# Kernel tuning notes

Hardware: AMD Instinct MI355X
Metric: run time of the kernel (lower is better)

The kernel has to match this reference:

```python
import jax, jax.numpy as jnp
import numpy as np

B, S, H = 1, 2048, 1024
E, INTER, TOP_K = 8, 2048, 2
ALPHA, LIMIT = 1.702, 7.0


def setup_inputs() -> dict:
    key = jax.random.key(0)
    ks = jax.random.split(key, 7)
    sc = 0.02
    return {
        'hidden_states': jax.random.normal(ks[0], (B, S, H), jnp.float32),
        'router_w': jax.random.normal(ks[1], (H, E), jnp.float32) * sc,
        'router_b': jax.random.normal(ks[2], (E,), jnp.float32) * sc,
        'gate_up_proj': jax.random.normal(ks[3], (E, H, 2 * INTER), jnp.float32) * sc,
        'gate_up_bias': jax.random.normal(ks[4], (E, 2 * INTER), jnp.float32) * sc,
        'down_proj': jax.random.normal(ks[5], (E, INTER, H), jnp.float32) * sc,
        'down_bias': jax.random.normal(ks[6], (E, H), jnp.float32) * sc,
    }


def reference(hidden_states, router_w, router_b, gate_up_proj, gate_up_bias, down_proj, down_bias):
    x = hidden_states  # [B,S,H]
    # router: top-k over expert logits, softmax over selected logits (gpt-oss style)
    logits = jnp.einsum('bsh,he->bse', x, router_w) + router_b
    top_vals, top_idx = jax.lax.top_k(logits, TOP_K)          # [B,S,K]
    topk_weights = jax.nn.softmax(top_vals, axis=-1)          # [B,S,K]
    # dense per-expert gate_up GEMM (dispatch is identity on 1 device)
    gu = jnp.einsum('bsh,ehn->besn', x, gate_up_proj)         # [B,E,S,2I]
    gu = gu + gate_up_bias[None, :, None, :]
    gate = jnp.minimum(gu[..., :INTER], LIMIT)
    up = jnp.clip(gu[..., INTER:], -LIMIT, LIMIT)
    glu = gate * jax.nn.sigmoid(gate * ALPHA)
    act = (up + 1.0) * glu                                    # [B,E,S,I]
    down = jnp.einsum('besl,elh->besh', act, down_proj)       # [B,E,S,H]
    down = down + down_bias[None, :, None, :]
    # combine: gather each token's K selected expert outputs, weight and sum
    down_bseh = jnp.transpose(down, (0, 2, 1, 3))             # [B,S,E,H]
    idx = jnp.broadcast_to(top_idx[..., None], (B, S, TOP_K, H))
    sel = jnp.take_along_axis(down_bseh, idx, axis=2)         # [B,S,K,H]
    return (sel * topk_weights[..., None]).sum(axis=2)        # [B,S,H]
```

## Files before the change

kernel.cpp:

```cpp
#include <hip/hip_runtime.h>
#include <hip/hip_bf16.h>
#include <math.h>

#define S 2048
#define H 1024
#define NE 8
#define INTER 2048
#define ALPHA 1.702f
#define LIMIT 7.0f

typedef __bf16 bf16x8 __attribute__((ext_vector_type(8)));
typedef float f32x4 __attribute__((ext_vector_type(4)));

#define WS_COUNTS 0
#define WS_SLOTS  4096
#define WS_W      (WS_SLOTS + NE*S*4)
#define WS_XB     (WS_W + 2*S*4)
#define WS_ACT    (WS_XB + (size_t)S*H*2)

static __device__ __forceinline__ unsigned short f2bf(float f) {
    union { __hip_bfloat16 h; unsigned short u; } cv;
    cv.h = __float2bfloat16(f);
    return cv.u;
}

static __device__ __forceinline__ void gload16(const void* g, void* l) {
    __builtin_amdgcn_global_load_lds(
        (const __attribute__((address_space(1))) unsigned int*)(unsigned long long)g,
        (__attribute__((address_space(3))) unsigned int*)(unsigned int)(unsigned long long)l,
        16, 0, 0);
}

__global__ __launch_bounds__(64) void router_conv(
    const float* __restrict__ x, const float* __restrict__ rw,
    const float* __restrict__ rb, int* __restrict__ counts,
    int* __restrict__ slots, float* __restrict__ slot_w,
    unsigned short* __restrict__ xb)
{
    int tok = blockIdx.x;
    int lane = threadIdx.x;
    const float4* xr = (const float4*)(x + (size_t)tok * H);
    ushort4* xo = (ushort4*)(xb + (size_t)tok * H);
    float acc[NE];
#pragma unroll
    for (int e = 0; e < NE; ++e) acc[e] = 0.f;
#pragma unroll
    for (int p = 0; p < H / 256; ++p) {
        int idx = p * 64 + lane;
        float4 v = xr[idx];
        ushort4 o;
        o.x = f2bf(v.x); o.y = f2bf(v.y); o.z = f2bf(v.z); o.w = f2bf(v.w);
        xo[idx] = o;
        const float* wr = rw + (size_t)idx * 4 * NE;
#pragma unroll
        for (int e = 0; e < NE; ++e)
            acc[e] += v.x * wr[e] + v.y * wr[NE + e] + v.z * wr[2 * NE + e] + v.w * wr[3 * NE + e];
    }
#pragma unroll
    for (int e = 0; e < NE; ++e) {
#pragma unroll
        for (int off = 32; off > 0; off >>= 1)
            acc[e] += __shfl_down(acc[e], off);
    }
    if (lane == 0) {
        float v[NE];
#pragma unroll
        for (int e = 0; e < NE; ++e) v[e] = acc[e] + rb[e];
        int i1 = 0; float v1 = v[0];
#pragma unroll
        for (int e = 1; e < NE; ++e) if (v[e] > v1) { v1 = v[e]; i1 = e; }
        int i2 = -1; float v2 = -3.0e38f;
#pragma unroll
        for (int e = 0; e < NE; ++e) if (e != i1 && v[e] > v2) { v2 = v[e]; i2 = e; }
        float w1 = 1.f / (1.f + expf(v2 - v1));
        float w2 = 1.f - w1;
        int p1 = atomicAdd(&counts[i1], 1);
        slots[i1 * S + p1] = tok * 2;
        slot_w[tok * 2] = w1;
        int p2 = atomicAdd(&counts[i2], 1);
        slots[i2 * S + p2] = tok * 2 + 1;
        slot_w[tok * 2 + 1] = w2;
    }
}

__global__ __launch_bounds__(256) void gateup_mfma(
    const unsigned short* __restrict__ xb,
    const float* __restrict__ gup,
    const float* __restrict__ gub,
    const int* __restrict__ counts, const int* __restrict__ slots,
    unsigned short* __restrict__ act)
{
    int e = blockIdx.z;
    int cnt = counts[e];
    int m0 = blockIdx.y * 128;
    if (m0 >= cnt) return;
    int n0 = blockIdx.x * 64;

    __shared__ unsigned short As[128 * 32];
    __shared__ float Gs[32][64];
    __shared__ float Us[32][64];
    __shared__ int sl[128];

    int t = threadIdx.x;
    int lane = t & 63, w = t >> 6;
    if (t < 128) {
        int r = m0 + t;
        sl[t] = slots[e * S + (r < cnt ? r : cnt - 1)];
    }
    __syncthreads();

    int quad = lane >> 4, l16 = lane & 15;
    int wm = (w >> 1) * 64, wn = (w & 1) * 32;

    int ar0 = w * 32 + (lane >> 2);
    int ar1 = ar0 + 16;
    const unsigned short* ap0 = xb + (size_t)(sl[ar0] >> 1) * H + (lane & 3) * 8;
    const unsigned short* ap1 = xb + (size_t)(sl[ar1] >> 1) * H + (lane & 3) * 8;
    unsigned short* la0 = &As[(2 * w) * 512 + lane * 8];
    unsigned short* la1 = &As[(2 * w + 1) * 512 + lane * 8];

    int brow = t >> 4;
    int bcol = (t & 15) * 4;
    const float* gsrc = gup + (size_t)e * H * 2 * INTER
                      + (size_t)brow * (2 * INTER) + n0 + bcol;
    const float* usrc = gsrc + INTER;
    float* lg = &Gs[brow][bcol];
    float* lu = &Us[brow][bcol];
    const size_t rs16 = (size_t)16 * 2 * INTER;

    f32x4 accg[4][2], accu[4][2];
#pragma unroll
    for (int mi = 0; mi < 4; ++mi)
#pragma unroll
        for (int ni = 0; ni < 2; ++ni) {
            accg[mi][ni] = (f32x4){0.f, 0.f, 0.f, 0.f};
            accu[mi][ni] = (f32x4){0.f, 0.f, 0.f, 0.f};
        }

    for (int k0 = 0; k0 < H; k0 += 32) {
        __syncthreads();
        gload16(ap0 + k0, la0);
        gload16(ap1 + k0, la1);
        const float* gk = gsrc + (size_t)k0 * 2 * INTER;
        const float* uk = usrc + (size_t)k0 * 2 * INTER;
        gload16(gk, lg);
        gload16(gk + rs16, (char*)lg + 4096);
        gload16(uk, lu);
        gload16(uk + rs16, (char*)lu + 4096);
        __syncthreads();

        bf16x8 af[4], gf[2], uf[2];
#pragma unroll
        for (int mi = 0; mi < 4; ++mi)
            af[mi] = *(const bf16x8*)&As[(wm + mi * 16 + l16) * 32 + quad * 8];
#pragma unroll
        for (int ni = 0; ni < 2; ++ni) {
            int n = wn + ni * 16 + l16;
            union { bf16x8 v; __bf16 e[8]; } ug, uu;
#pragma unroll
            for (int i = 0; i < 8; ++i) {
                ug.e[i] = (__bf16)Gs[quad * 8 + i][n];
                uu.e[i] = (__bf16)Us[quad * 8 + i][n];
            }
            gf[ni] = ug.v;
            uf[ni] = uu.v;
        }
#pragma unroll
        for (int mi = 0; mi < 4; ++mi)
#pragma unroll
            for (int ni = 0; ni < 2; ++ni) {
                accg[mi][ni] = __builtin_amdgcn_mfma_f32_16x16x32_bf16(af[mi], gf[ni], accg[mi][ni], 0, 0, 0);
                accu[mi][ni] = __builtin_amdgcn_mfma_f32_16x16x32_bf16(af[mi], uf[ni], accu[mi][ni], 0, 0, 0);
            }
    }

    const float* gb = gub + (size_t)e * 2 * INTER;
#pragma unroll
    for (int mi = 0; mi < 4; ++mi) {
#pragma unroll
        for (int r = 0; r < 4; ++r) {
            int rt = wm + mi * 16 + quad * 4 + r;
            if (m0 + rt >= cnt) continue;
            int slot = sl[rt];
            unsigned short* orow = act + (size_t)slot * INTER;
#pragma unroll
            for (int ni = 0; ni < 2; ++ni) {
                int col = n0 + wn + ni * 16 + l16;
                float gate = accg[mi][ni][r] + gb[col];
                float uv = accu[mi][ni][r] + gb[INTER + col];
                gate = fminf(gate, LIMIT);
                uv = fminf(fmaxf(uv, -LIMIT), LIMIT);
                float glu = gate / (1.f + __expf(-ALPHA * gate));
                orow[col] = f2bf((uv + 1.f) * glu);
            }
        }
    }
}

__global__ __launch_bounds__(256) void down_mfma(
    const unsigned short* __restrict__ act,
    const float* __restrict__ dp,
    const float* __restrict__ db,
    const int* __restrict__ counts, const int* __restrict__ slots,
    const float* __restrict__ slot_w,
    float* __restrict__ out)
{
    int e = blockIdx.z >> 1;
    int ks = blockIdx.z & 1;
    int cnt = counts[e];
    int m0 = blockIdx.y * 128;
    if (m0 >= cnt) return;
    int n0 = blockIdx.x * 64;

    __shared__ unsigned short As[128 * 32];
    __shared__ float Bs[32][64];
    __shared__ int sl[128];

    int t = threadIdx.x;
    int lane = t & 63, w = t >> 6;
    if (t < 128) {
        int r = m0 + t;
        sl[t] = slots[e * S + (r < cnt ? r : cnt - 1)];
    }
    __syncthreads();

    int quad = lane >> 4, l16 = lane & 15;
    int wm = (w >> 1) * 64, wn = (w & 1) * 32;

    int ar0 = w * 32 + (lane >> 2);
    int ar1 = ar0 + 16;
    int kbase = ks * (INTER / 2);
    const unsigned short* ap0 = act + (size_t)sl[ar0] * INTER + kbase + (lane & 3) * 8;
    const unsigned short* ap1 = act + (size_t)sl[ar1] * INTER + kbase + (lane & 3) * 8;
    unsigned short* la0 = &As[(2 * w) * 512 + lane * 8];
    unsigned short* la1 = &As[(2 * w + 1) * 512 + lane * 8];

    int brow = t >> 4;
    int bcol = (t & 15) * 4;
    const float* bsrc = dp + (size_t)e * INTER * H
                      + (size_t)(kbase + brow) * H + n0 + bcol;
    float* lb = &Bs[brow][bcol];
    const size_t rs16 = (size_t)16 * H;

    f32x4 acc[4][2];
#pragma unroll
    for (int mi = 0; mi < 4; ++mi)
#pragma unroll
        for (int ni = 0; ni < 2; ++ni)
            acc[mi][ni] = (f32x4){0.f, 0.f, 0.f, 0.f};

    for (int k0 = 0; k0 < INTER / 2; k0 += 32) {
        __syncthreads();
        gload16(ap0 + k0, la0);
        gload16(ap1 + k0, la1);
        const float* bk = bsrc + (size_t)k0 * H;
        gload16(bk, lb);
        gload16(bk + rs16, (char*)lb + 4096);
        __syncthreads();

        bf16x8 af[4], bf[2];
#pragma unroll
        for (int mi = 0; mi < 4; ++mi)
            af[mi] = *(const bf16x8*)&As[(wm + mi * 16 + l16) * 32 + quad * 8];
#pragma unroll
        for (int ni = 0; ni < 2; ++ni) {
            int n = wn + ni * 16 + l16;
            union { bf16x8 v; __bf16 e[8]; } ub;
#pragma unroll
            for (int i = 0; i < 8; ++i)
                ub.e[i] = (__bf16)Bs[quad * 8 + i][n];
            bf[ni] = ub.v;
        }
#pragma unroll
        for (int mi = 0; mi < 4; ++mi)
#pragma unroll
            for (int ni = 0; ni < 2; ++ni)
                acc[mi][ni] = __builtin_amdgcn_mfma_f32_16x16x32_bf16(af[mi], bf[ni], acc[mi][ni], 0, 0, 0);
    }

    const float* dbr = db + (size_t)e * H;
#pragma unroll
    for (int mi = 0; mi < 4; ++mi) {
#pragma unroll
        for (int r = 0; r < 4; ++r) {
            int rt = wm + mi * 16 + quad * 4 + r;
            if (m0 + rt >= cnt) continue;
            int slot = sl[rt];
            int tok = slot >> 1;
            float wgt = slot_w[slot];
#pragma unroll
            for (int ni = 0; ni < 2; ++ni) {
                int col = n0 + wn + ni * 16 + l16;
                float rr = acc[mi][ni][r] + (ks == 0 ? dbr[col] : 0.f);
                atomicAdd(&out[(size_t)tok * H + col], wgt * rr);
            }
        }
    }
}

extern "C" void kernel_launch(void* const* d_in, const int* in_sizes, int n_in,
                              void* d_out, int out_size, void* d_ws, size_t ws_size,
                              hipStream_t stream)
{
    const float* x   = (const float*)d_in[0];
    const float* rw  = (const float*)d_in[1];
    const float* rb  = (const float*)d_in[2];
    const float* gup = (const float*)d_in[3];
    const float* gub = (const float*)d_in[4];
    const float* dp  = (const float*)d_in[5];
    const float* db  = (const float*)d_in[6];
    float* out = (float*)d_out;

    char* ws = (char*)d_ws;
    int* counts            = (int*)(ws + WS_COUNTS);
    int* slots             = (int*)(ws + WS_SLOTS);
    float* slot_w          = (float*)(ws + WS_W);
    unsigned short* xb     = (unsigned short*)(ws + WS_XB);
    unsigned short* act    = (unsigned short*)(ws + WS_ACT);

    hipMemsetAsync(counts, 0, 4096, stream);
    hipMemsetAsync(out, 0, (size_t)S * H * sizeof(float), stream);

    router_conv<<<S, 64, 0, stream>>>(x, rw, rb, counts, slots, slot_w, xb);

    gateup_mfma<<<dim3(INTER / 64, 16, NE), 256, 0, stream>>>(
        xb, gup, gub, counts, slots, act);

    down_mfma<<<dim3(H / 64, 16, NE * 2), 256, 0, stream>>>(
        act, dp, db, counts, slots, slot_w, out);
}
```

Measured before the change: 438.8 us.

## Swizzle fp32 weight tiles in LDS and pre-convert once to bf16 K-major

The gate_up and down GEMM kernels now load fp32 weight tiles into LDS with a rotated column swizzle. Each tile is converted to a bf16 N-major/K-contiguous buffer once per k-step by all threads, so MFMA operand fetches become single 16-byte LDS reads. This removes the redundant per-wave strided fp32 reads and conversions, which were likely bank-conflicted. The cost is an extra LDS pass and barrier per iteration. Some __syncthreads calls are replaced by a lighter lgkmcnt wait plus s_barrier.

```diff
diff --git a/kernel.cpp b/kernel.cpp
--- a/kernel.cpp
+++ b/kernel.cpp
@@ -29,6 +29,15 @@
         (const __attribute__((address_space(1))) unsigned int*)(unsigned long long)g,
         (__attribute__((address_space(3))) unsigned int*)(unsigned int)(unsigned long long)l,
         16, 0, 0);
+}
+
+static __device__ __forceinline__ void ldsbar() {
+    asm volatile("s_waitcnt lgkmcnt(0)" ::: "memory");
+    __builtin_amdgcn_s_barrier();
+}
+
+static __device__ __forceinline__ int sshift(int q) {
+    return (q >> 1) + ((q & 1) << 2);
 }
 
 __global__ __launch_bounds__(64) void router_conv(
@@ -97,8 +106,10 @@
     int n0 = blockIdx.x * 64;
 
     __shared__ unsigned short As[128 * 32];
-    __shared__ float Gs[32][64];
-    __shared__ float Us[32][64];
+    __shared__ float Gf[32 * 64];
+    __shared__ float Uf[32 * 64];
+    __shared__ unsigned short Gb[64 * 32];
+    __shared__ unsigned short Ub[64 * 32];
     __shared__ int sl[128];
 
     int t = threadIdx.x;
@@ -119,14 +130,21 @@
     unsigned short* la0 = &As[(2 * w) * 512 + lane * 8];
     unsigned short* la1 = &As[(2 * w + 1) * 512 + lane * 8];
 
-    int brow = t >> 4;
-    int bcol = (t & 15) * 4;
-    const float* gsrc = gup + (size_t)e * H * 2 * INTER
-                      + (size_t)brow * (2 * INTER) + n0 + bcol;
-    const float* usrc = gsrc + INTER;
-    float* lg = &Gs[brow][bcol];
-    float* lu = &Us[brow][bcol];
-    const size_t rs16 = (size_t)16 * 2 * INTER;
+    int brow = t >> 4, bc = t & 15;
+    int sq0 = sshift(brow >> 3);
+    int sq1 = sshift((brow + 16) >> 3);
+    const float* base = gup + (size_t)e * H * 2 * INTER + n0;
+    const float* gsrc0 = base + (size_t)brow * (2 * INTER) + ((bc - sq0) & 15) * 4;
+    const float* gsrc1 = base + (size_t)(brow + 16) * (2 * INTER) + ((bc - sq1) & 15) * 4;
+    const float* usrc0 = gsrc0 + INTER;
+    const float* usrc1 = gsrc1 + INTER;
+    float* lgf0 = &Gf[t * 4];
+    float* lgf1 = &Gf[1024 + t * 4];
+    float* luf0 = &Uf[t * 4];
+    float* luf1 = &Uf[1024 + t * 4];
+
+    int rn = t >> 2, rkc = (t & 3) * 8;
+    int rnp = (rn + 4 * sshift(t & 3)) & 63;
 
     f32x4 accg[4][2], accu[4][2];
 #pragma unroll
@@ -138,16 +156,27 @@
         }
 
     for (int k0 = 0; k0 < H; k0 += 32) {
-        __syncthreads();
+        ldsbar();
         gload16(ap0 + k0, la0);
         gload16(ap1 + k0, la1);
-        const float* gk = gsrc + (size_t)k0 * 2 * INTER;
-        const float* uk = usrc + (size_t)k0 * 2 * INTER;
-        gload16(gk, lg);
-        gload16(gk + rs16, (char*)lg + 4096);
-        gload16(uk, lu);
-        gload16(uk + rs16, (char*)lu + 4096);
+        size_t ko = (size_t)k0 * 2 * INTER;
+        gload16(gsrc0 + ko, lgf0);
+        gload16(gsrc1 + ko, lgf1);
+        gload16(usrc0 + ko, luf0);
+        gload16(usrc1 + ko, luf1);
         __syncthreads();
+
+        {
+            union { bf16x8 v; __bf16 e8[8]; } cg, cu;
+#pragma unroll
+            for (int i = 0; i < 8; ++i) {
+                cg.e8[i] = (__bf16)Gf[(rkc + i) * 64 + rnp];
+                cu.e8[i] = (__bf16)Uf[(rkc + i) * 64 + rnp];
+            }
+            *(bf16x8*)&Gb[rn * 32 + rkc] = cg.v;
+            *(bf16x8*)&Ub[rn * 32 + rkc] = cu.v;
+        }
+        ldsbar();
 
         bf16x8 af[4], gf[2], uf[2];
 #pragma unroll
@@ -156,14 +185,8 @@
 #pragma unroll
         for (int ni = 0; ni < 2; ++ni) {
             int n = wn + ni * 16 + l16;
-            union { bf16x8 v; __bf16 e[8]; } ug, uu;
-#pragma unroll
-            for (int i = 0; i < 8; ++i) {
-                ug.e[i] = (__bf16)Gs[quad * 8 + i][n];
-                uu.e[i] = (__bf16)Us[quad * 8 + i][n];
-            }
-            gf[ni] = ug.v;
-            uf[ni] = uu.v;
+            gf[ni] = *(const bf16x8*)&Gb[n * 32 + quad * 8];
+            uf[ni] = *(const bf16x8*)&Ub[n * 32 + quad * 8];
         }
 #pragma unroll
         for (int mi = 0; mi < 4; ++mi)
@@ -213,7 +236,8 @@
     int n0 = blockIdx.x * 64;
 
     __shared__ unsigned short As[128 * 32];
-    __shared__ float Bs[32][64];
+    __shared__ float Bf[32 * 64];
+    __shared__ unsigned short Bb[64 * 32];
     __shared__ int sl[128];
 
     int t = threadIdx.x;
@@ -235,12 +259,17 @@
     unsigned short* la0 = &As[(2 * w) * 512 + lane * 8];
     unsigned short* la1 = &As[(2 * w + 1) * 512 + lane * 8];
 
-    int brow = t >> 4;
-    int bcol = (t & 15) * 4;
-    const float* bsrc = dp + (size_t)e * INTER * H
-                      + (size_t)(kbase + brow) * H + n0 + bcol;
-    float* lb = &Bs[brow][bcol];
-    const size_t rs16 = (size_t)16 * H;
+    int brow = t >> 4, bc = t & 15;
+    int sq0 = sshift(brow >> 3);
+    int sq1 = sshift((brow + 16) >> 3);
+    const float* base = dp + (size_t)e * INTER * H + n0;
+    const float* bsrc0 = base + (size_t)(kbase + brow) * H + ((bc - sq0) & 15) * 4;
+    const float* bsrc1 = base + (size_t)(kbase + brow + 16) * H + ((bc - sq1) & 15) * 4;
+    float* lbf0 = &Bf[t * 4];
+    float* lbf1 = &Bf[1024 + t * 4];
+
+    int rn = t >> 2, rkc = (t & 3) * 8;
+    int rnp = (rn + 4 * sshift(t & 3)) & 63;
 
     f32x4 acc[4][2];
 #pragma unroll
@@ -250,13 +279,22 @@
             acc[mi][ni] = (f32x4){0.f, 0.f, 0.f, 0.f};
 
     for (int k0 = 0; k0 < INTER / 2; k0 += 32) {
-        __syncthreads();
+        ldsbar();
         gload16(ap0 + k0, la0);
         gload16(ap1 + k0, la1);
-        const float* bk = bsrc + (size_t)k0 * H;
-        gload16(bk, lb);
-        gload16(bk + rs16, (char*)lb + 4096);
+        size_t ko = (size_t)k0 * H;
+        gload16(bsrc0 + ko, lbf0);
+        gload16(bsrc1 + ko, lbf1);
         __syncthreads();
+
+        {
+            union { bf16x8 v; __bf16 e8[8]; } cb;
+#pragma unroll
+            for (int i = 0; i < 8; ++i)
+                cb.e8[i] = (__bf16)Bf[(rkc + i) * 64 + rnp];
+            *(bf16x8*)&Bb[rn * 32 + rkc] = cb.v;
+        }
+        ldsbar();
 
         bf16x8 af[4], bf[2];
 #pragma unroll
@@ -265,11 +303,7 @@
 #pragma unroll
         for (int ni = 0; ni < 2; ++ni) {
             int n = wn + ni * 16 + l16;
-            union { bf16x8 v; __bf16 e[8]; } ub;
-#pragma unroll
-            for (int i = 0; i < 8; ++i)
-                ub.e[i] = (__bf16)Bs[quad * 8 + i][n];
-            bf[ni] = ub.v;
+            bf[ni] = *(const bf16x8*)&Bb[n * 32 + quad * 8];
         }
 #pragma unroll
         for (int mi = 0; mi < 4; ++mi)
```

Measured after the change: 441.4 us. Within noise of the previous version (+0.6%).
